# Kernel tuning notes

Measured on AMD Instinct MI355X. Metric: run time of the kernel, lower is better.

## Reference

```python
import jax, jax.numpy as jnp
import numpy as np

NUM_EDGE_TYPES = 4
TIME_STEPS = (1, 1)  # one propagation step per layer, 2 layers
HIDDEN = 128
N_NODES = 50000
N_EDGES = 400000


def setup_inputs() -> dict:
    key = jax.random.key(0)
    ks = jax.random.split(key, 8)
    states = jax.random.normal(ks[0], (N_NODES, HIDDEN), jnp.float32)
    etype = jax.random.randint(ks[1], (N_EDGES,), 0, NUM_EDGE_TYPES, jnp.int32)
    src = jax.random.randint(ks[2], (N_EDGES,), 0, N_NODES, jnp.int32)
    dst = jax.random.randint(ks[3], (N_EDGES,), 0, N_NODES, jnp.int32)
    edges = jnp.stack([etype, src, dst], axis=-1)  # [E, 3] = (type, src, dst)
    L = len(TIME_STEPS)
    std = HIDDEN ** -0.5  # matches tf.random_normal_initializer(stddev=H**-0.5)
    type_W = jax.random.normal(ks[4], (L, NUM_EDGE_TYPES, HIDDEN, HIDDEN), jnp.float32) * std
    type_b = jax.random.normal(ks[5], (L, NUM_EDGE_TYPES, HIDDEN), jnp.float32) * std
    gru_kernel = jax.random.normal(ks[6], (L, HIDDEN, 3 * HIDDEN), jnp.float32) * std
    gru_rkernel = jax.random.normal(ks[7], (L, HIDDEN, 3 * HIDDEN), jnp.float32) * std
    gru_bias = jnp.zeros((L, 2, 3 * HIDDEN), jnp.float32)  # [input_bias, recurrent_bias]
    return dict(states=states, edges=edges, type_W=type_W, type_b=type_b,
                gru_kernel=gru_kernel, gru_rkernel=gru_rkernel, gru_bias=gru_bias)


def _gru_cell(x, h, kernel, rkernel, bias):
    # tf.keras.layers.GRUCell with defaults (reset_after=True, sigmoid/tanh)
    mx = x @ kernel + bias[0]   # [N, 3H]
    mh = h @ rkernel + bias[1]  # [N, 3H]
    xz, xr, xh = jnp.split(mx, 3, axis=-1)
    hz, hr, hh = jnp.split(mh, 3, axis=-1)
    z = jax.nn.sigmoid(xz + hz)
    r = jax.nn.sigmoid(xr + hr)
    c = jnp.tanh(xh + r * hh)
    return z * h + (1.0 - z) * c


def _propagate(h, layer_no, edges, type_W, type_b):
    etype, src, dst = edges[:, 0], edges[:, 1], edges[:, 2]
    src_states = h[src]  # [E, H] irregular gather
    msgs = jnp.zeros_like(src_states)
    # per-edge-type dense transform, combined via masking (jit-friendly
    # equivalent of tf.dynamic_partition + per-type matmul)
    for t in range(NUM_EDGE_TYPES):
        mt = src_states @ type_W[layer_no, t] + type_b[layer_no, t]
        msgs = msgs + jnp.where((etype == t)[:, None], mt, 0.0)
    # scatter-add messages into destination nodes
    return jax.ops.segment_sum(msgs, dst, num_segments=h.shape[0])


def reference(states, edges, type_W, type_b, gru_kernel, gru_rkernel, gru_bias):
    h = states
    for layer_no, steps in enumerate(TIME_STEPS):
        for _ in range(steps):
            agg = _propagate(h, layer_no, edges, type_W, type_b)
            h = _gru_cell(agg, h, gru_kernel[layer_no], gru_rkernel[layer_no], gru_bias[layer_no])
    return h
```

## Files before the change

### kernel.cpp

```cpp
#include <hip/hip_runtime.h>
#include <hip/hip_bf16.h>

#define H 128
#define NT 4
#define CAP4 40
#define BK 64

typedef __attribute__((ext_vector_type(8))) _Float16 half8;
typedef __attribute__((ext_vector_type(4))) float f32x4;

#if defined(__has_builtin)
#if __has_builtin(__builtin_amdgcn_global_load_lds)
#define HAS_GLL 1
#endif
#endif
#ifndef HAS_GLL
#define HAS_GLL 0
#endif

__device__ __forceinline__ float bf2f(unsigned short u) {
    union { unsigned int i; float f; } v;
    v.i = ((unsigned int)u) << 16;
    return v.f;
}

__device__ __forceinline__ unsigned short f2bf(float f) {
    union { float f; unsigned int i; } v;
    v.f = f;
    unsigned int x = v.i;
    unsigned int r = (x + 0x7fffu + ((x >> 16) & 1u)) >> 16;
    return (unsigned short)r;
}

__device__ __forceinline__ float fsigmoid(float x) {
    return 1.0f / (1.0f + __expf(-x));
}
__device__ __forceinline__ float ftanh(float x) {
    return 1.0f - 2.0f / (__expf(2.0f * x) + 1.0f);
}

__device__ __forceinline__ float readf(const void* p, long i, int isbf) {
    return isbf ? bf2f(((const unsigned short*)p)[i]) : ((const float*)p)[i];
}

__device__ __forceinline__ void gll16(const _Float16* g, _Float16* l) {
#if HAS_GLL
    __builtin_amdgcn_global_load_lds(
        (const __attribute__((address_space(1))) unsigned int*)g,
        (__attribute__((address_space(3))) unsigned int*)l, 16, 0, 0);
#endif
}

template<int RPW>
__device__ __forceinline__ void stage_tileT(
    const _Float16* __restrict__ gbase, int rstride, int row0, int kof,
    int maxrow, _Float16* lds) {
    const int wave = threadIdx.x >> 6, lane = threadIdx.x & 63;
#pragma unroll
    for (int s = 0; s < RPW / 8; s++) {
        int R = wave * RPW + s * 8;
        int rl = R + (lane >> 3);
        int rg = row0 + rl;
        if (rg >= maxrow) rg = maxrow - 1;
        int chunk = (lane & 7) ^ (rl & 7);
        const _Float16* gp = gbase + (size_t)rg * rstride + kof + chunk * 8;
#if HAS_GLL
        gll16(gp, lds + R * 64);
#else
        *(half8*)&lds[rl * 64 + (lane & 7) * 8] = *(const half8*)gp;
#endif
    }
}

__device__ __forceinline__ half8 frag(const _Float16* lds, int r, int g) {
    return *(const half8*)&lds[r * 64 + ((g ^ (r & 7)) * 8)];
}

__global__ void detect_dtype(const unsigned short* __restrict__ states_u16,
                             int* __restrict__ flag) {
    __shared__ int cnt;
    if (threadIdx.x == 0) cnt = 0;
    __syncthreads();
    int local = 0;
    for (int i = threadIdx.x; i < 1024; i += 256) {
        unsigned short u = states_u16[2 * i];
        int e = (u >> 7) & 0xFF;
        if (e >= 96 && e <= 158) local++;
    }
    atomicAdd(&cnt, local);
    __syncthreads();
    if (threadIdx.x == 0) *flag = (cnt >= 512) ? 1 : 0;
}

__global__ void prep_all(
    const void* __restrict__ states, const void* __restrict__ type_W,
    const void* __restrict__ type_b, const void* __restrict__ gk,
    const void* __restrict__ gr, const void* __restrict__ grub,
    _Float16* __restrict__ h16, _Float16* __restrict__ BTw,
    _Float16* __restrict__ BTg, float* __restrict__ btab,
    float* __restrict__ gbsum, float* __restrict__ gb0c,
    float* __restrict__ gb1c, int* __restrict__ counts4,
    const int* __restrict__ flag,
    long NNH, int nBTw, int nBTg, int NC4, int LAYERS) {
    long i = (long)blockIdx.x * 256 + threadIdx.x;
    const int fl = *flag;
    if (i < NNH) {
        h16[i] = (_Float16)readf(states, i, fl);
        return;
    }
    i -= NNH;
    if (i < nBTw) {
        int l = (int)(i >> 16);
        int rem = (int)(i & 65535);
        int c = rem >> 9, kk = rem & 511;
        int t = kk >> 7, k = kk & 127;
        BTw[i] = (_Float16)readf(type_W, (((long)(l * NT + t) * H) + k) * H + c, fl);
        return;
    }
    i -= nBTw;
    if (i < nBTg) {
        int l = (int)(i >> 17);
        int rem = (int)(i & 131071);
        int nc = rem >> 8, k = rem & 255;
        int g = nc >> 6, gate = (nc >> 4) & 3, m = nc & 15;
        int c = g * 16 + m;
        float v = 0.0f;
        if (gate == 0) {
            v = (k < 128) ? readf(gk, ((long)l * H + k) * 384 + c, fl)
                          : readf(gr, ((long)l * H + (k - 128)) * 384 + c, fl);
        } else if (gate == 1) {
            v = (k < 128) ? readf(gk, ((long)l * H + k) * 384 + 128 + c, fl)
                          : readf(gr, ((long)l * H + (k - 128)) * 384 + 128 + c, fl);
        } else if (gate == 2) {
            if (k < 128) v = readf(gk, ((long)l * H + k) * 384 + 256 + c, fl);
        } else {
            if (k >= 128) v = readf(gr, ((long)l * H + (k - 128)) * 384 + 256 + c, fl);
        }
        BTg[i] = (_Float16)v;
        return;
    }
    i -= nBTg;
    if (i < NC4) {
        counts4[i] = 0;
        return;
    }
    i -= NC4;
    {
        int j = (int)i;
        if (j < LAYERS * NT * H) btab[j] = readf(type_b, j, fl);
        if (j < LAYERS * 256) {
            int l = j >> 8, c = j & 255;
            gbsum[j] = readf(grub, (long)l * 768 + c, fl) +
                       readf(grub, (long)l * 768 + 384 + c, fl);
        }
        if (j < LAYERS * H) {
            int l = j >> 7, c = j & 127;
            gb0c[j] = readf(grub, (long)l * 768 + 256 + c, fl);
            gb1c[j] = readf(grub, (long)l * 768 + 384 + 256 + c, fl);
        }
    }
}

__global__ void place_edges4(const int* __restrict__ edges, int* __restrict__ counts4,
                             int* __restrict__ buckets4, int NE) {
    int e = blockIdx.x * 256 + threadIdx.x;
    if (e >= NE) return;
    int t = edges[3 * e], src = edges[3 * e + 1], dst = edges[3 * e + 2];
    int slot = atomicAdd(&counts4[dst * 4 + t], 1);
    if (slot < CAP4) buckets4[((size_t)dst * 4 + t) * CAP4 + slot] = src;
}

__global__ __launch_bounds__(256) void gather4(
    const _Float16* __restrict__ h16, const int* __restrict__ counts4,
    const int* __restrict__ buckets4, _Float16* __restrict__ A4, int NN) {
    int node = blockIdx.x * 4 + (threadIdx.x >> 6);
    int lane = threadIdx.x & 63;
    int q = lane >> 4, i = lane & 15;
    if (node >= NN) return;
    int cnt = counts4[node * 4 + q];
    if (cnt > CAP4) cnt = CAP4;
    const int* bkt = buckets4 + ((size_t)node * 4 + q) * CAP4;

    float acc[8] = {};
    int e = 0;
    for (; e + 2 <= cnt; e += 2) {
        int s0 = bkt[e], s1 = bkt[e + 1];
        half8 v0 = *(const half8*)&h16[(size_t)s0 * H + i * 8];
        half8 v1 = *(const half8*)&h16[(size_t)s1 * H + i * 8];
#pragma unroll
        for (int j = 0; j < 8; j++) acc[j] += (float)v0[j] + (float)v1[j];
    }
    if (e < cnt) {
        int s0 = bkt[e];
        half8 v0 = *(const half8*)&h16[(size_t)s0 * H + i * 8];
#pragma unroll
        for (int j = 0; j < 8; j++) acc[j] += (float)v0[j];
    }

    half8 o;
#pragma unroll
    for (int j = 0; j < 8; j++) o[j] = (_Float16)acc[j];
    *(half8*)&A4[((size_t)node * 4 + q) * H + i * 8] = o;
}

__global__ __launch_bounds__(256, 4) void layer_fused(
    const _Float16* __restrict__ A4,
    const _Float16* __restrict__ h16,
    const _Float16* __restrict__ BTw,
    const _Float16* __restrict__ BTg,
    const float* __restrict__ btab,
    const int4* __restrict__ cnt4,
    const float* __restrict__ gbsum,
    const float* __restrict__ gb0c,
    const float* __restrict__ gb1c,
    _Float16* __restrict__ hnext,
    void* __restrict__ outbuf,
    const int* __restrict__ flag, int NN) {
    __shared__ _Float16 scratch[12288];
    __shared__ _Float16 aggL[8192];

    const int row0 = blockIdx.x * 64;
    const int tid = threadIdx.x;
    const int wave = tid >> 6, lane = tid & 63;
    const int m = lane & 15, quad = lane >> 4;
    const int wr = (wave & 1) * 32, wc = (wave >> 1) * 64;

    f32x4 acc[2][4] = {};

    for (int kc = 0; kc < 8; kc++) {
        const int k0 = kc * BK;
        __syncthreads();
        stage_tileT<16>(A4, 512, row0, k0, NN, scratch);
        stage_tileT<32>(BTw, 512, 0, k0, 128, scratch + 4096);
        __syncthreads();
#pragma unroll
        for (int ks = 0; ks < 2; ks++) {
            half8 a[2], b[4];
#pragma unroll
            for (int mt = 0; mt < 2; mt++)
                a[mt] = frag(scratch, wr + mt * 16 + m, ks * 4 + quad);
#pragma unroll
            for (int nt = 0; nt < 4; nt++)
                b[nt] = frag(scratch + 4096, wc + nt * 16 + m, ks * 4 + quad);
#pragma unroll
            for (int mt = 0; mt < 2; mt++)
#pragma unroll
                for (int nt = 0; nt < 4; nt++)
                    acc[mt][nt] = __builtin_amdgcn_mfma_f32_16x16x32_f16(
                        a[mt], b[nt], acc[mt][nt], 0, 0, 0);
        }
    }

#pragma unroll
    for (int mt = 0; mt < 2; mt++) {
#pragma unroll
        for (int i = 0; i < 4; i++) {
            int rl = wr + mt * 16 + quad * 4 + i;
            int rg = row0 + rl;
            if (rg >= NN) rg = NN - 1;
            int4 c4 = cnt4[rg];
#pragma unroll
            for (int nt = 0; nt < 4; nt++) {
                int c = wc + nt * 16 + m;
                float bias = c4.x * btab[c] + c4.y * btab[128 + c] +
                             c4.z * btab[256 + c] + c4.w * btab[384 + c];
                int tile = c >> 6, cc = c & 63, g = cc >> 3;
                aggL[tile * 4096 + rl * 64 + ((g ^ (rl & 7)) * 8) + (cc & 7)] =
                    (_Float16)(acc[mt][nt][i] + bias);
            }
        }
    }

    const int fl = outbuf ? *flag : 0;
    for (int y = 0; y < 4; y++) {
#pragma unroll
        for (int mt = 0; mt < 2; mt++)
#pragma unroll
            for (int nt = 0; nt < 4; nt++)
                acc[mt][nt] = (f32x4){0.f, 0.f, 0.f, 0.f};

        for (int kc = 0; kc < 4; kc++) {
            const int ntA = (kc < 2) ? 2 : 3;
            __syncthreads();
            stage_tileT<32>(BTg, 256, y * 128, kc * BK, 512, scratch);
            if (kc >= 2)
                stage_tileT<16>(h16, H, row0, (kc - 2) * BK, NN, scratch + 8192);
            __syncthreads();
#pragma unroll
            for (int ks = 0; ks < 2; ks++) {
                const _Float16* Asrc =
                    (kc < 2) ? (aggL + kc * 4096) : (scratch + 8192);
                half8 a[2], b3[3];
#pragma unroll
                for (int mt = 0; mt < 2; mt++)
                    a[mt] = frag(Asrc, wr + mt * 16 + m, ks * 4 + quad);
                b3[0] = frag(scratch, wc + 0 * 16 + m, ks * 4 + quad);
                b3[1] = frag(scratch, wc + 1 * 16 + m, ks * 4 + quad);
                b3[2] = frag(scratch, wc + ntA * 16 + m, ks * 4 + quad);
#pragma unroll
                for (int mt = 0; mt < 2; mt++) {
                    acc[mt][0] = __builtin_amdgcn_mfma_f32_16x16x32_f16(
                        a[mt], b3[0], acc[mt][0], 0, 0, 0);
                    acc[mt][1] = __builtin_amdgcn_mfma_f32_16x16x32_f16(
                        a[mt], b3[1], acc[mt][1], 0, 0, 0);
                    acc[mt][ntA] = __builtin_amdgcn_mfma_f32_16x16x32_f16(
                        a[mt], b3[2], acc[mt][ntA], 0, 0, 0);
                }
            }
        }

        const int g8 = y * 2 + (wc >> 6);
        const int c = g8 * 16 + m;
        const float bz = gbsum[c];
        const float br = gbsum[128 + c];
        const float bx = gb0c[c];
        const float bh = gb1c[c];
#pragma unroll
        for (int mt = 0; mt < 2; mt++) {
#pragma unroll
            for (int i = 0; i < 4; i++) {
                int rl = wr + mt * 16 + quad * 4 + i;
                int row = row0 + rl;
                if (row >= NN) continue;
                float z = fsigmoid(acc[mt][0][i] + bz);
                float r = fsigmoid(acc[mt][1][i] + br);
                float ccand =
                    ftanh((acc[mt][2][i] + bx) + r * (acc[mt][3][i] + bh));
                float hv = (float)h16[(size_t)row * H + c];
                float hn = z * hv + (1.0f - z) * ccand;
                size_t oi = (size_t)row * H + c;
                hnext[oi] = (_Float16)hn;
                if (outbuf) {
                    if (fl) ((unsigned short*)outbuf)[oi] = f2bf(hn);
                    else    ((float*)outbuf)[oi] = hn;
                }
            }
        }
    }
}

extern "C" void kernel_launch(void* const* d_in, const int* in_sizes, int n_in,
                              void* d_out, int out_size, void* d_ws, size_t ws_size,
                              hipStream_t stream) {
    const void* states = d_in[0];
    const int*  edges  = (const int*)d_in[1];
    const void* type_W = d_in[2];
    const void* type_b = d_in[3];
    const void* gruk   = d_in[4];
    const void* grur   = d_in[5];
    const void* grub   = d_in[6];

    const int NN = in_sizes[0] / H;
    const int NE = in_sizes[1] / 3;
    const int nW = in_sizes[2];
    const int LAYERS = nW / (NT * H * H);

    char* w = (char*)d_ws;
    int* flag = (int*)w;                               w += 64;
    _Float16* h16A  = (_Float16*)w;                    w += (size_t)NN * H * 2;
    _Float16* h16B  = (_Float16*)w;                    w += (size_t)NN * H * 2;
    _Float16* A4    = (_Float16*)w;                    w += (size_t)NN * 4 * H * 2;
    _Float16* BTw = (_Float16*)w;                      w += (size_t)LAYERS * H * 512 * 2;
    _Float16* BTg = (_Float16*)w;                      w += (size_t)LAYERS * 512 * 256 * 2;
    float* btab  = (float*)w;                          w += (size_t)LAYERS * NT * H * 4;
    float* gbsum = (float*)w;                          w += (size_t)LAYERS * 256 * 4;
    float* gb0c  = (float*)w;                          w += (size_t)LAYERS * H * 4;
    float* gb1c  = (float*)w;                          w += (size_t)LAYERS * H * 4;
    int* counts4 = (int*)w;                            w += (size_t)NN * 4 * 4;
    int* buckets4 = (int*)w;

    detect_dtype<<<1, 256, 0, stream>>>((const unsigned short*)states, flag);

    const long NNH = (long)NN * H;
    const int nBTw = LAYERS * 65536;
    const int nBTg = LAYERS * 131072;
    const int NC4 = NN * 4;
    const long ptotal = NNH + nBTw + nBTg + NC4 + LAYERS * NT * H;
    prep_all<<<(int)((ptotal + 255) / 256), 256, 0, stream>>>(
        states, type_W, type_b, gruk, grur, grub,
        h16A, BTw, BTg, btab, gbsum, gb0c, gb1c, counts4, flag,
        NNH, nBTw, nBTg, NC4, LAYERS);

    place_edges4<<<(NE + 255) / 256, 256, 0, stream>>>(edges, counts4, buckets4, NE);

    const int rt64 = (NN + 63) / 64;
    for (int L = 0; L < LAYERS; L++) {
        const _Float16* hcur = (L & 1) ? h16B : h16A;
        _Float16* hnext      = (L & 1) ? h16A : h16B;

        gather4<<<(NN + 3) / 4, 256, 0, stream>>>(hcur, counts4, buckets4, A4, NN);

        layer_fused<<<rt64, 256, 0, stream>>>(
            A4, hcur,
            BTw + (size_t)L * H * 512,
            BTg + (size_t)L * 512 * 256,
            btab + (size_t)L * NT * H, (const int4*)counts4,
            gbsum + (size_t)L * 256, gb0c + (size_t)L * H, gb1c + (size_t)L * H,
            hnext, (L == LAYERS - 1) ? d_out : nullptr, flag, NN);
    }
}
```

Before: 277.7 us.

## Fuse per-type neighbor gather into layer kernel and read weights directly from global

Removes the separate gather4 kernel and the A4 intermediate by having each block gather its 64 nodes' per-type neighbor sums directly into LDS, two edge types per pass. Weight fragments for both GEMMs and the h operand are now loaded straight from global memory instead of being staged through LDS. Output is staged through LDS so hnext and the final output can be written with vector stores. This saves a launch and a large intermediate round-trip, but puts the irregular gather latency inside the MFMA kernel, lowers occupancy (launch bounds 3 and more LDS), and relies on cache hits for the repeated weight reads.

```diff
diff --git a/kernel.cpp b/kernel.cpp
--- a/kernel.cpp
+++ b/kernel.cpp
@@ -4,19 +4,10 @@
 #define H 128
 #define NT 4
 #define CAP4 40
-#define BK 64
 
 typedef __attribute__((ext_vector_type(8))) _Float16 half8;
+typedef __attribute__((ext_vector_type(8))) unsigned short ushort8;
 typedef __attribute__((ext_vector_type(4))) float f32x4;
-
-#if defined(__has_builtin)
-#if __has_builtin(__builtin_amdgcn_global_load_lds)
-#define HAS_GLL 1
-#endif
-#endif
-#ifndef HAS_GLL
-#define HAS_GLL 0
-#endif
 
 __device__ __forceinline__ float bf2f(unsigned short u) {
     union { unsigned int i; float f; } v;
@@ -41,35 +32,6 @@
 
 __device__ __forceinline__ float readf(const void* p, long i, int isbf) {
     return isbf ? bf2f(((const unsigned short*)p)[i]) : ((const float*)p)[i];
-}
-
-__device__ __forceinline__ void gll16(const _Float16* g, _Float16* l) {
-#if HAS_GLL
-    __builtin_amdgcn_global_load_lds(
-        (const __attribute__((address_space(1))) unsigned int*)g,
-        (__attribute__((address_space(3))) unsigned int*)l, 16, 0, 0);
-#endif
-}
-
-template<int RPW>
-__device__ __forceinline__ void stage_tileT(
-    const _Float16* __restrict__ gbase, int rstride, int row0, int kof,
-    int maxrow, _Float16* lds) {
-    const int wave = threadIdx.x >> 6, lane = threadIdx.x & 63;
-#pragma unroll
-    for (int s = 0; s < RPW / 8; s++) {
-        int R = wave * RPW + s * 8;
-        int rl = R + (lane >> 3);
-        int rg = row0 + rl;
-        if (rg >= maxrow) rg = maxrow - 1;
-        int chunk = (lane & 7) ^ (rl & 7);
-        const _Float16* gp = gbase + (size_t)rg * rstride + kof + chunk * 8;
-#if HAS_GLL
-        gll16(gp, lds + R * 64);
-#else
-        *(half8*)&lds[rl * 64 + (lane & 7) * 8] = *(const half8*)gp;
-#endif
-    }
 }
 
 __device__ __forceinline__ half8 frag(const _Float16* lds, int r, int g) {
@@ -170,53 +132,22 @@
     if (slot < CAP4) buckets4[((size_t)dst * 4 + t) * CAP4 + slot] = src;
 }
 
-__global__ __launch_bounds__(256) void gather4(
-    const _Float16* __restrict__ h16, const int* __restrict__ counts4,
-    const int* __restrict__ buckets4, _Float16* __restrict__ A4, int NN) {
-    int node = blockIdx.x * 4 + (threadIdx.x >> 6);
-    int lane = threadIdx.x & 63;
-    int q = lane >> 4, i = lane & 15;
-    if (node >= NN) return;
-    int cnt = counts4[node * 4 + q];
-    if (cnt > CAP4) cnt = CAP4;
-    const int* bkt = buckets4 + ((size_t)node * 4 + q) * CAP4;
-
-    float acc[8] = {};
-    int e = 0;
-    for (; e + 2 <= cnt; e += 2) {
-        int s0 = bkt[e], s1 = bkt[e + 1];
-        half8 v0 = *(const half8*)&h16[(size_t)s0 * H + i * 8];
-        half8 v1 = *(const half8*)&h16[(size_t)s1 * H + i * 8];
-#pragma unroll
-        for (int j = 0; j < 8; j++) acc[j] += (float)v0[j] + (float)v1[j];
-    }
-    if (e < cnt) {
-        int s0 = bkt[e];
-        half8 v0 = *(const half8*)&h16[(size_t)s0 * H + i * 8];
-#pragma unroll
-        for (int j = 0; j < 8; j++) acc[j] += (float)v0[j];
-    }
-
-    half8 o;
-#pragma unroll
-    for (int j = 0; j < 8; j++) o[j] = (_Float16)acc[j];
-    *(half8*)&A4[((size_t)node * 4 + q) * H + i * 8] = o;
-}
-
-__global__ __launch_bounds__(256, 4) void layer_fused(
-    const _Float16* __restrict__ A4,
+__global__ __launch_bounds__(256, 3) void layer_fused(
     const _Float16* __restrict__ h16,
+    const int* __restrict__ counts4,
+    const int* __restrict__ buckets4,
     const _Float16* __restrict__ BTw,
     const _Float16* __restrict__ BTg,
     const float* __restrict__ btab,
-    const int4* __restrict__ cnt4,
     const float* __restrict__ gbsum,
     const float* __restrict__ gb0c,
     const float* __restrict__ gb1c,
     _Float16* __restrict__ hnext,
     void* __restrict__ outbuf,
     const int* __restrict__ flag, int NN) {
-    __shared__ _Float16 scratch[12288];
+    __shared__ __align__(16) char ubuf[33792];
+    _Float16* As = (_Float16*)ubuf;
+    float* hout = (float*)ubuf;
     __shared__ _Float16 aggL[8192];
 
     const int row0 = blockIdx.x * 64;
@@ -224,30 +155,68 @@
     const int wave = tid >> 6, lane = tid & 63;
     const int m = lane & 15, quad = lane >> 4;
     const int wr = (wave & 1) * 32, wc = (wave >> 1) * 64;
+    const int4* cnt4 = (const int4*)counts4;
 
     f32x4 acc[2][4] = {};
 
-    for (int kc = 0; kc < 8; kc++) {
-        const int k0 = kc * BK;
+    for (int pass = 0; pass < 2; pass++) {
+        if (pass) __syncthreads();
+        {
+            const int sub = lane >> 4, i = lane & 15;
+            const int nodeoff = sub >> 1, tloc = sub & 1;
+            const int t = pass * 2 + tloc;
+            for (int jn = 0; jn < 8; jn++) {
+                int rl = wave * 16 + jn * 2 + nodeoff;
+                int node = row0 + rl;
+                float acg[8] = {};
+                if (node < NN) {
+                    int cnt = counts4[node * 4 + t];
+                    if (cnt > CAP4) cnt = CAP4;
+                    const int* bkt = buckets4 + ((size_t)node * 4 + t) * CAP4;
+                    int e = 0;
+                    for (; e + 2 <= cnt; e += 2) {
+                        int s0 = bkt[e], s1 = bkt[e + 1];
+                        half8 v0 = *(const half8*)&h16[(size_t)s0 * H + i * 8];
+                        half8 v1 = *(const half8*)&h16[(size_t)s1 * H + i * 8];
+#pragma unroll
+                        for (int k = 0; k < 8; k++)
+                            acg[k] += (float)v0[k] + (float)v1[k];
+                    }
+                    if (e < cnt) {
+                        int s0 = bkt[e];
+                        half8 v0 = *(const half8*)&h16[(size_t)s0 * H + i * 8];
+#pragma unroll
+                        for (int k = 0; k < 8; k++) acg[k] += (float)v0[k];
+                    }
+                }
+                half8 o;
+#pragma unroll
+                for (int k = 0; k < 8; k++) o[k] = (_Float16)acg[k];
+                *(half8*)&As[(tloc * 2 + (i >> 3)) * 4096 + rl * 64 +
+                             (((i & 7) ^ (rl & 7)) * 8)] = o;
+            }
+        }
         __syncthreads();
-        stage_tileT<16>(A4, 512, row0, k0, NN, scratch);
-        stage_tileT<32>(BTw, 512, 0, k0, 128, scratch + 4096);
-        __syncthreads();
-#pragma unroll
-        for (int ks = 0; ks < 2; ks++) {
-            half8 a[2], b[4];
-#pragma unroll
-            for (int mt = 0; mt < 2; mt++)
-                a[mt] = frag(scratch, wr + mt * 16 + m, ks * 4 + quad);
-#pragma unroll
-            for (int nt = 0; nt < 4; nt++)
-                b[nt] = frag(scratch + 4096, wc + nt * 16 + m, ks * 4 + quad);
-#pragma unroll
-            for (int mt = 0; mt < 2; mt++)
+#pragma unroll
+        for (int kcl = 0; kcl < 4; kcl++) {
+            const int k0 = pass * 256 + kcl * 64;
+#pragma unroll
+            for (int ks = 0; ks < 2; ks++) {
+                half8 a[2], b[4];
+#pragma unroll
+                for (int mt = 0; mt < 2; mt++)
+                    a[mt] = frag(As + kcl * 4096, wr + mt * 16 + m, ks * 4 + quad);
 #pragma unroll
                 for (int nt = 0; nt < 4; nt++)
-                    acc[mt][nt] = __builtin_amdgcn_mfma_f32_16x16x32_f16(
-                        a[mt], b[nt], acc[mt][nt], 0, 0, 0);
+                    b[nt] = *(const half8*)&BTw[(size_t)(wc + nt * 16 + m) * 512 +
+                                                k0 + (ks * 4 + quad) * 8];
+#pragma unroll
+                for (int mt = 0; mt < 2; mt++)
+#pragma unroll
+                    for (int nt = 0; nt < 4; nt++)
+                        acc[mt][nt] = __builtin_amdgcn_mfma_f32_16x16x32_f16(
+                            a[mt], b[nt], acc[mt][nt], 0, 0, 0);
+            }
         }
     }
 
@@ -270,41 +239,46 @@
             }
         }
     }
+    __syncthreads();
 
     const int fl = outbuf ? *flag : 0;
     for (int y = 0; y < 4; y++) {
-#pragma unroll
-        for (int mt = 0; mt < 2; mt++)
-#pragma unroll
-            for (int nt = 0; nt < 4; nt++)
-                acc[mt][nt] = (f32x4){0.f, 0.f, 0.f, 0.f};
-
+        f32x4 p[2][4] = {};
+#pragma unroll
         for (int kc = 0; kc < 4; kc++) {
             const int ntA = (kc < 2) ? 2 : 3;
-            __syncthreads();
-            stage_tileT<32>(BTg, 256, y * 128, kc * BK, 512, scratch);
-            if (kc >= 2)
-                stage_tileT<16>(h16, H, row0, (kc - 2) * BK, NN, scratch + 8192);
-            __syncthreads();
 #pragma unroll
             for (int ks = 0; ks < 2; ks++) {
-                const _Float16* Asrc =
-                    (kc < 2) ? (aggL + kc * 4096) : (scratch + 8192);
                 half8 a[2], b3[3];
-#pragma unroll
-                for (int mt = 0; mt < 2; mt++)
-                    a[mt] = frag(Asrc, wr + mt * 16 + m, ks * 4 + quad);
-                b3[0] = frag(scratch, wc + 0 * 16 + m, ks * 4 + quad);
-                b3[1] = frag(scratch, wc + 1 * 16 + m, ks * 4 + quad);
-                b3[2] = frag(scratch, wc + ntA * 16 + m, ks * 4 + quad);
+                if (kc < 2) {
+#pragma unroll
+                    for (int mt = 0; mt < 2; mt++)
+                        a[mt] = frag(aggL + kc * 4096, wr + mt * 16 + m,
+                                     ks * 4 + quad);
+                } else {
+#pragma unroll
+                    for (int mt = 0; mt < 2; mt++) {
+                        int rg = row0 + wr + mt * 16 + m;
+                        if (rg >= NN) rg = NN - 1;
+                        a[mt] = *(const half8*)&h16[(size_t)rg * H +
+                                                    (kc - 2) * 64 +
+                                                    (ks * 4 + quad) * 8];
+                    }
+                }
+                b3[0] = *(const half8*)&BTg[(size_t)(y * 128 + wc + m) * 256 +
+                                            kc * 64 + (ks * 4 + quad) * 8];
+                b3[1] = *(const half8*)&BTg[(size_t)(y * 128 + wc + 16 + m) * 256 +
+                                            kc * 64 + (ks * 4 + quad) * 8];
+                b3[2] = *(const half8*)&BTg[(size_t)(y * 128 + wc + ntA * 16 + m) * 256 +
+                                            kc * 64 + (ks * 4 + quad) * 8];
 #pragma unroll
                 for (int mt = 0; mt < 2; mt++) {
-                    acc[mt][0] = __builtin_amdgcn_mfma_f32_16x16x32_f16(
-                        a[mt], b3[0], acc[mt][0], 0, 0, 0);
-                    acc[mt][1] = __builtin_amdgcn_mfma_f32_16x16x32_f16(
-                        a[mt], b3[1], acc[mt][1], 0, 0, 0);
-                    acc[mt][ntA] = __builtin_amdgcn_mfma_f32_16x16x32_f16(
-                        a[mt], b3[2], acc[mt][ntA], 0, 0, 0);
+                    p[mt][0] = __builtin_amdgcn_mfma_f32_16x16x32_f16(
+                        a[mt], b3[0], p[mt][0], 0, 0, 0);
+                    p[mt][1] = __builtin_amdgcn_mfma_f32_16x16x32_f16(
+                        a[mt], b3[1], p[mt][1], 0, 0, 0);
+                    p[mt][ntA] = __builtin_amdgcn_mfma_f32_16x16x32_f16(
+                        a[mt], b3[2], p[mt][ntA], 0, 0, 0);
                 }
             }
         }
@@ -320,20 +294,54 @@
 #pragma unroll
             for (int i = 0; i < 4; i++) {
                 int rl = wr + mt * 16 + quad * 4 + i;
-                int row = row0 + rl;
-                if (row >= NN) continue;
-                float z = fsigmoid(acc[mt][0][i] + bz);
-                float r = fsigmoid(acc[mt][1][i] + br);
+                int rg = row0 + rl;
+                if (rg >= NN) rg = NN - 1;
+                float z = fsigmoid(p[mt][0][i] + bz);
+                float r = fsigmoid(p[mt][1][i] + br);
                 float ccand =
-                    ftanh((acc[mt][2][i] + bx) + r * (acc[mt][3][i] + bh));
-                float hv = (float)h16[(size_t)row * H + c];
-                float hn = z * hv + (1.0f - z) * ccand;
-                size_t oi = (size_t)row * H + c;
-                hnext[oi] = (_Float16)hn;
-                if (outbuf) {
-                    if (fl) ((unsigned short*)outbuf)[oi] = f2bf(hn);
-                    else    ((float*)outbuf)[oi] = hn;
+                    ftanh((p[mt][2][i] + bx) + r * (p[mt][3][i] + bh));
+                float hv = (float)h16[(size_t)rg * H + c];
+                hout[rl * 132 + c] = z * hv + (1.0f - z) * ccand;
+            }
+        }
+    }
+    __syncthreads();
+
+#pragma unroll
+    for (int rep = 0; rep < 2; rep++) {
+        int idx = rep * 256 + tid;
+        int r = idx >> 3, s = idx & 7;
+        int row = row0 + r;
+        if (row >= NN) continue;
+        float v[16];
+#pragma unroll
+        for (int k = 0; k < 16; k++) v[k] = hout[r * 132 + s * 16 + k];
+        half8 h0, h1;
+#pragma unroll
+        for (int k = 0; k < 8; k++) {
+            h0[k] = (_Float16)v[k];
+            h1[k] = (_Float16)v[8 + k];
+        }
+        size_t o = (size_t)row * H + s * 16;
+        *(half8*)&hnext[o] = h0;
+        *(half8*)&hnext[o + 8] = h1;
+        if (outbuf) {
+            if (fl) {
+                ushort8 u0, u1;
+#pragma unroll
+                for (int k = 0; k < 8; k++) {
+                    u0[k] = f2bf(v[k]);
+                    u1[k] = f2bf(v[8 + k]);
                 }
+                unsigned short* ob = (unsigned short*)outbuf + o;
+                *(ushort8*)&ob[0] = u0;
+                *(ushort8*)&ob[8] = u1;
+            } else {
+                float* ob = (float*)outbuf + o;
+#pragma unroll
+                for (int k = 0; k < 4; k++)
+                    *(f32x4*)&ob[k * 4] = (f32x4){v[k * 4], v[k * 4 + 1],
+                                                  v[k * 4 + 2], v[k * 4 + 3]};
             }
         }
     }
@@ -359,7 +367,6 @@
     int* flag = (int*)w;                               w += 64;
     _Float16* h16A  = (_Float16*)w;                    w += (size_t)NN * H * 2;
     _Float16* h16B  = (_Float16*)w;                    w += (size_t)NN * H * 2;
-    _Float16* A4    = (_Float16*)w;                    w += (size_t)NN * 4 * H * 2;
     _Float16* BTw = (_Float16*)w;                      w += (size_t)LAYERS * H * 512 * 2;
     _Float16* BTg = (_Float16*)w;                      w += (size_t)LAYERS * 512 * 256 * 2;
     float* btab  = (float*)w;                          w += (size_t)LAYERS * NT * H * 4;
@@ -388,13 +395,11 @@
         const _Float16* hcur = (L & 1) ? h16B : h16A;
         _Float16* hnext      = (L & 1) ? h16A : h16B;
 
-        gather4<<<(NN + 3) / 4, 256, 0, stream>>>(hcur, counts4, buckets4, A4, NN);
-
         layer_fused<<<rt64, 256, 0, stream>>>(
-            A4, hcur,
+            hcur, counts4, buckets4,
             BTw + (size_t)L * H * 512,
             BTg + (size_t)L * 512 * 256,
-            btab + (size_t)L * NT * H, (const int4*)counts4,
+            btab + (size_t)L * NT * H,
             gbsum + (size_t)L * 256, gb0c + (size_t)L * H, gb1c + (size_t)L * H,
             hnext, (L == LAYERS - 1) ? d_out : nullptr, flag, NN);
     }
```

Result: slower. 428.6 us (+54.4%).

## Pre-swizzle weights for direct global fragment loads and double-buffer A tiles

Applied to the files above, without the earlier changes.

Weights are repacked so each MFMA B fragment can be read straight from global/L2 memory, dropping their LDS staging. The A4 tile is double-buffered in LDS, removing one barrier per k-step. The h tile is staged into LDS once and reused for both the GRU matmul and the blend, and hnext is written through LDS with coalesced vector stores. The gather loop is unrolled to four edges and occupancy is lowered to 3 blocks. The cost is more LDS per block and repeated global weight reads that depend on cache hits.

```diff
diff --git a/kernel.cpp b/kernel.cpp
--- a/kernel.cpp
+++ b/kernel.cpp
@@ -4,9 +4,9 @@
 #define H 128
 #define NT 4
 #define CAP4 40
-#define BK 64
 
 typedef __attribute__((ext_vector_type(8))) _Float16 half8;
+typedef __attribute__((ext_vector_type(8))) unsigned short ushort8;
 typedef __attribute__((ext_vector_type(4))) float f32x4;
 
 #if defined(__has_builtin)
@@ -51,14 +51,13 @@
 #endif
 }
 
-template<int RPW>
-__device__ __forceinline__ void stage_tileT(
+__device__ __forceinline__ void stage64(
     const _Float16* __restrict__ gbase, int rstride, int row0, int kof,
     int maxrow, _Float16* lds) {
     const int wave = threadIdx.x >> 6, lane = threadIdx.x & 63;
 #pragma unroll
-    for (int s = 0; s < RPW / 8; s++) {
-        int R = wave * RPW + s * 8;
+    for (int s = 0; s < 2; s++) {
+        int R = wave * 16 + s * 8;
         int rl = R + (lane >> 3);
         int rg = row0 + rl;
         if (rg >= maxrow) rg = maxrow - 1;
@@ -111,19 +110,31 @@
     i -= NNH;
     if (i < nBTw) {
         int l = (int)(i >> 16);
-        int rem = (int)(i & 65535);
-        int c = rem >> 9, kk = rem & 511;
-        int t = kk >> 7, k = kk & 127;
-        BTw[i] = (_Float16)readf(type_W, (((long)(l * NT + t) * H) + k) * H + c, fl);
+        int r16 = (int)(i & 65535);
+        int cblk = r16 >> 13;
+        int rem = r16 & 8191;
+        int g = rem >> 7;
+        int mm = (rem >> 3) & 15;
+        int j = rem & 7;
+        int c = cblk * 16 + mm;
+        int k = g * 8 + j;
+        int t = k >> 7, kk = k & 127;
+        BTw[i] = (_Float16)readf(type_W, (((long)(l * NT + t) * H) + kk) * H + c, fl);
         return;
     }
     i -= nBTw;
     if (i < nBTg) {
         int l = (int)(i >> 17);
-        int rem = (int)(i & 131071);
-        int nc = rem >> 8, k = rem & 255;
-        int g = nc >> 6, gate = (nc >> 4) & 3, m = nc & 15;
-        int c = g * 16 + m;
+        int r17 = (int)(i & 131071);
+        int ncblk = r17 >> 12;
+        int rem = r17 & 4095;
+        int g = rem >> 7;
+        int mm = (rem >> 3) & 15;
+        int j = rem & 7;
+        int nc = ncblk * 16 + mm;
+        int k = g * 8 + j;
+        int gblk = nc >> 6, gate = (nc >> 4) & 3;
+        int c = gblk * 16 + (nc & 15);
         float v = 0.0f;
         if (gate == 0) {
             v = (k < 128) ? readf(gk, ((long)l * H + k) * 384 + c, fl)
@@ -183,12 +194,23 @@
 
     float acc[8] = {};
     int e = 0;
-    for (; e + 2 <= cnt; e += 2) {
+    for (; e + 4 <= cnt; e += 4) {
+        int s0 = bkt[e], s1 = bkt[e + 1], s2 = bkt[e + 2], s3 = bkt[e + 3];
+        half8 v0 = *(const half8*)&h16[(size_t)s0 * H + i * 8];
+        half8 v1 = *(const half8*)&h16[(size_t)s1 * H + i * 8];
+        half8 v2 = *(const half8*)&h16[(size_t)s2 * H + i * 8];
+        half8 v3 = *(const half8*)&h16[(size_t)s3 * H + i * 8];
+#pragma unroll
+        for (int j = 0; j < 8; j++)
+            acc[j] += ((float)v0[j] + (float)v1[j]) + ((float)v2[j] + (float)v3[j]);
+    }
+    if (e + 2 <= cnt) {
         int s0 = bkt[e], s1 = bkt[e + 1];
         half8 v0 = *(const half8*)&h16[(size_t)s0 * H + i * 8];
         half8 v1 = *(const half8*)&h16[(size_t)s1 * H + i * 8];
 #pragma unroll
         for (int j = 0; j < 8; j++) acc[j] += (float)v0[j] + (float)v1[j];
+        e += 2;
     }
     if (e < cnt) {
         int s0 = bkt[e];
@@ -203,7 +225,7 @@
     *(half8*)&A4[((size_t)node * 4 + q) * H + i * 8] = o;
 }
 
-__global__ __launch_bounds__(256, 4) void layer_fused(
+__global__ __launch_bounds__(256, 3) void layer_fused(
     const _Float16* __restrict__ A4,
     const _Float16* __restrict__ h16,
     const _Float16* __restrict__ BTw,
@@ -216,7 +238,8 @@
     _Float16* __restrict__ hnext,
     void* __restrict__ outbuf,
     const int* __restrict__ flag, int NN) {
-    __shared__ _Float16 scratch[12288];
+    __shared__ __align__(16) _Float16 Asd[8192];
+    __shared__ _Float16 hL[8192];
     __shared__ _Float16 aggL[8192];
 
     const int row0 = blockIdx.x * 64;
@@ -227,21 +250,23 @@
 
     f32x4 acc[2][4] = {};
 
+    stage64(A4, 512, row0, 0, NN, Asd);
+    __syncthreads();
     for (int kc = 0; kc < 8; kc++) {
-        const int k0 = kc * BK;
-        __syncthreads();
-        stage_tileT<16>(A4, 512, row0, k0, NN, scratch);
-        stage_tileT<32>(BTw, 512, 0, k0, 128, scratch + 4096);
-        __syncthreads();
+        const _Float16* cur = Asd + (kc & 1) * 4096;
+        if (kc < 7) stage64(A4, 512, row0, (kc + 1) * 64, NN,
+                            Asd + ((kc + 1) & 1) * 4096);
 #pragma unroll
         for (int ks = 0; ks < 2; ks++) {
+            const int gk = kc * 8 + ks * 4 + quad;
             half8 a[2], b[4];
 #pragma unroll
             for (int mt = 0; mt < 2; mt++)
-                a[mt] = frag(scratch, wr + mt * 16 + m, ks * 4 + quad);
+                a[mt] = frag(cur, wr + mt * 16 + m, ks * 4 + quad);
 #pragma unroll
             for (int nt = 0; nt < 4; nt++)
-                b[nt] = frag(scratch + 4096, wc + nt * 16 + m, ks * 4 + quad);
+                b[nt] = *(const half8*)&BTw[(((size_t)((wc >> 4) + nt)) << 13) +
+                                            gk * 128 + m * 8];
 #pragma unroll
             for (int mt = 0; mt < 2; mt++)
 #pragma unroll
@@ -249,7 +274,11 @@
                     acc[mt][nt] = __builtin_amdgcn_mfma_f32_16x16x32_f16(
                         a[mt], b[nt], acc[mt][nt], 0, 0, 0);
         }
-    }
+        __syncthreads();
+    }
+
+    stage64(h16, H, row0, 0, NN, hL);
+    stage64(h16, H, row0, 64, NN, hL + 4096);
 
 #pragma unroll
     for (int mt = 0; mt < 2; mt++) {
@@ -270,41 +299,39 @@
             }
         }
     }
+    __syncthreads();
+    _Float16* hout16 = Asd;
 
     const int fl = outbuf ? *flag : 0;
     for (int y = 0; y < 4; y++) {
-#pragma unroll
-        for (int mt = 0; mt < 2; mt++)
-#pragma unroll
-            for (int nt = 0; nt < 4; nt++)
-                acc[mt][nt] = (f32x4){0.f, 0.f, 0.f, 0.f};
-
+        f32x4 p[2][4] = {};
+#pragma unroll
         for (int kc = 0; kc < 4; kc++) {
             const int ntA = (kc < 2) ? 2 : 3;
-            __syncthreads();
-            stage_tileT<32>(BTg, 256, y * 128, kc * BK, 512, scratch);
-            if (kc >= 2)
-                stage_tileT<16>(h16, H, row0, (kc - 2) * BK, NN, scratch + 8192);
-            __syncthreads();
+            const _Float16* Asrc = (kc < 2) ? (aggL + kc * 4096)
+                                            : (hL + (kc - 2) * 4096);
 #pragma unroll
             for (int ks = 0; ks < 2; ks++) {
-                const _Float16* Asrc =
-                    (kc < 2) ? (aggL + kc * 4096) : (scratch + 8192);
+                const int gk = kc * 8 + ks * 4 + quad;
                 half8 a[2], b3[3];
 #pragma unroll
                 for (int mt = 0; mt < 2; mt++)
                     a[mt] = frag(Asrc, wr + mt * 16 + m, ks * 4 + quad);
-                b3[0] = frag(scratch, wc + 0 * 16 + m, ks * 4 + quad);
-                b3[1] = frag(scratch, wc + 1 * 16 + m, ks * 4 + quad);
-                b3[2] = frag(scratch, wc + ntA * 16 + m, ks * 4 + quad);
+                const int ncb = y * 8 + (wc >> 4);
+                b3[0] = *(const half8*)&BTg[(((size_t)(ncb + 0)) << 12) +
+                                            gk * 128 + m * 8];
+                b3[1] = *(const half8*)&BTg[(((size_t)(ncb + 1)) << 12) +
+                                            gk * 128 + m * 8];
+                b3[2] = *(const half8*)&BTg[(((size_t)(ncb + ntA)) << 12) +
+                                            gk * 128 + m * 8];
 #pragma unroll
                 for (int mt = 0; mt < 2; mt++) {
-                    acc[mt][0] = __builtin_amdgcn_mfma_f32_16x16x32_f16(
-                        a[mt], b3[0], acc[mt][0], 0, 0, 0);
-                    acc[mt][1] = __builtin_amdgcn_mfma_f32_16x16x32_f16(
-                        a[mt], b3[1], acc[mt][1], 0, 0, 0);
-                    acc[mt][ntA] = __builtin_amdgcn_mfma_f32_16x16x32_f16(
-                        a[mt], b3[2], acc[mt][ntA], 0, 0, 0);
+                    p[mt][0] = __builtin_amdgcn_mfma_f32_16x16x32_f16(
+                        a[mt], b3[0], p[mt][0], 0, 0, 0);
+                    p[mt][1] = __builtin_amdgcn_mfma_f32_16x16x32_f16(
+                        a[mt], b3[1], p[mt][1], 0, 0, 0);
+                    p[mt][ntA] = __builtin_amdgcn_mfma_f32_16x16x32_f16(
+                        a[mt], b3[2], p[mt][ntA], 0, 0, 0);
                 }
             }
         }
@@ -315,26 +342,47 @@
         const float br = gbsum[128 + c];
         const float bx = gb0c[c];
         const float bh = gb1c[c];
+        const int hsub = c >> 6, hcc = c & 63, hg = hcc >> 3, hj = hcc & 7;
 #pragma unroll
         for (int mt = 0; mt < 2; mt++) {
 #pragma unroll
             for (int i = 0; i < 4; i++) {
                 int rl = wr + mt * 16 + quad * 4 + i;
                 int row = row0 + rl;
-                if (row >= NN) continue;
-                float z = fsigmoid(acc[mt][0][i] + bz);
-                float r = fsigmoid(acc[mt][1][i] + br);
+                float z = fsigmoid(p[mt][0][i] + bz);
+                float r = fsigmoid(p[mt][1][i] + br);
                 float ccand =
-                    ftanh((acc[mt][2][i] + bx) + r * (acc[mt][3][i] + bh));
-                float hv = (float)h16[(size_t)row * H + c];
+                    ftanh((p[mt][2][i] + bx) + r * (p[mt][3][i] + bh));
+                float hv = (float)hL[hsub * 4096 + rl * 64 +
+                                     ((hg ^ (rl & 7)) * 8) + hj];
                 float hn = z * hv + (1.0f - z) * ccand;
-                size_t oi = (size_t)row * H + c;
-                hnext[oi] = (_Float16)hn;
                 if (outbuf) {
-                    if (fl) ((unsigned short*)outbuf)[oi] = f2bf(hn);
-                    else    ((float*)outbuf)[oi] = hn;
+                    if (row < NN) {
+                        size_t oi = (size_t)row * H + c;
+                        if (fl) ((unsigned short*)outbuf)[oi] = f2bf(hn);
+                        else    ((float*)outbuf)[oi] = hn;
+                    }
+                } else {
+                    hout16[rl * 128 + c] = (_Float16)hn;
                 }
             }
+        }
+    }
+
+    if (!outbuf) {
+        __syncthreads();
+        int r = tid >> 2, s = tid & 3;
+        int row = row0 + r;
+        if (row < NN) {
+            half8 v0 = *(const half8*)&hout16[r * 128 + s * 32];
+            half8 v1 = *(const half8*)&hout16[r * 128 + s * 32 + 8];
+            half8 v2 = *(const half8*)&hout16[r * 128 + s * 32 + 16];
+            half8 v3 = *(const half8*)&hout16[r * 128 + s * 32 + 24];
+            size_t o = (size_t)row * H + s * 32;
+            *(half8*)&hnext[o] = v0;
+            *(half8*)&hnext[o + 8] = v1;
+            *(half8*)&hnext[o + 16] = v2;
+            *(half8*)&hnext[o + 24] = v3;
         }
     }
 }
```

Result: slower. 297.8 us (+7.2%).
